# Optimization experiments

Measured on AMD Instinct MI355X. Metric: run time of the kernel, lower is better.

## Reference

```python
import math
import jax, jax.numpy as jnp
import numpy as np

WS = 16        # window size (square)
SHIFT = 8      # window_size // 2 (window_shift=True)
NUM_HEADS = 6

def _rel_coords_table(ws):
    # Swin-V2 log-spaced continuous relative coords, shape (1, 2ws-1, 2ws-1, 2)
    r = np.arange(-(ws - 1), ws, dtype=np.float32)
    t = np.stack(np.meshgrid(r, r, indexing='ij'), axis=-1)[None]
    t = t / (ws - 1) * 8.0
    t = np.sign(t) * np.log2(np.abs(t) + 1.0) / np.log2(8.0)
    return t.astype(np.float32)

def _rel_pos_index(ws):
    ch, cw = np.meshgrid(np.arange(ws), np.arange(ws), indexing='ij')
    coords = np.stack([ch.ravel(), cw.ravel()])          # (2, N)
    rel = coords[:, :, None] - coords[:, None, :]        # (2, N, N)
    rel = rel.transpose(1, 2, 0).astype(np.int64)
    rel[..., 0] += ws - 1
    rel[..., 1] += ws - 1
    rel[..., 0] *= 2 * ws - 1
    return rel.sum(-1).astype(np.int32)                  # (N, N), values in [0, (2ws-1)^2)

def _shift_mask(H, W, ws, shift):
    img = np.zeros((H, W), dtype=np.float32)
    cnt = 0
    for hs in (slice(0, -ws), slice(-ws, -shift), slice(-shift, None)):
        for wsl in (slice(0, -ws), slice(-ws, -shift), slice(-shift, None)):
            img[hs, wsl] = cnt; cnt += 1
    win = img.reshape(H // ws, ws, W // ws, ws).transpose(0, 2, 1, 3).reshape(-1, ws * ws)
    diff = win[:, None, :] - win[:, :, None]
    return np.where(diff != 0, -100.0, 0.0).astype(np.float32)  # (nW, N, N)

def setup_inputs():
    key = jax.random.key(0)
    ks = jax.random.split(key, 4)
    B, H, W = 16, 64, 64
    C = 3 * NUM_HEADS * 32  # 576 (qkv channels)
    qkv = jax.random.normal(ks[0], (B, H * W, C), dtype=jnp.float32)
    table = jnp.asarray(_rel_coords_table(WS))
    index = jnp.asarray(_rel_pos_index(WS))
    mask = jnp.asarray(_shift_mask(H, W, WS, SHIFT))
    logit_scale = jnp.log(10.0 * jnp.ones((NUM_HEADS, 1, 1), dtype=jnp.float32))
    w1 = jax.random.normal(ks[1], (512, 2), dtype=jnp.float32) * 0.02
    b1 = jnp.zeros((512,), dtype=jnp.float32)
    w2 = jax.random.normal(ks[2], (NUM_HEADS, 512), dtype=jnp.float32) * 0.02
    return {"qkv": qkv, "table": table, "mask": mask, "logit_scale": logit_scale,
            "w1": w1, "b1": b1, "w2": w2, "index": index, "H": H, "W": W}

def reference(qkv, table, mask, logit_scale, w1, b1, w2, index, H, W):
    B, L, C = qkv.shape
    dim = C // 3
    hd = dim // NUM_HEADS
    x = qkv.reshape(B, H, W, C)
    x = jnp.roll(x, (-SHIFT, -SHIFT), axis=(1, 2))
    nWh, nWw = H // WS, W // WS
    # window partition -> (B_, N, C)
    x = x.reshape(B, nWh, WS, nWw, WS, C).transpose(0, 1, 3, 2, 4, 5).reshape(-1, WS * WS, C)
    B_, N, _ = x.shape
    qkv_ = x.reshape(B_, N, 3, NUM_HEADS, hd).transpose(2, 0, 3, 1, 4)
    q, k, v = qkv_[0], qkv_[1], qkv_[2]  # (B_, H, N, hd)
    # cosine attention
    qn = q / jnp.maximum(jnp.linalg.norm(q, axis=-1, keepdims=True), 1e-12)
    kn = k / jnp.maximum(jnp.linalg.norm(k, axis=-1, keepdims=True), 1e-12)
    attn = jnp.einsum('bhnd,bhmd->bhnm', qn, kn)
    scale = jnp.exp(jnp.minimum(logit_scale, math.log(1.0 / 0.01)))  # (H,1,1)
    attn = attn * scale[None]
    # CPB MLP bias: Linear(2,512)+ReLU -> Linear(512,H,no bias)
    hidden = jax.nn.relu(table @ w1.T + b1)          # (1, 2ws-1, 2ws-1, 512)
    bias_table = (hidden @ w2.T).reshape(-1, NUM_HEADS)
    bias = bias_table[index.reshape(-1)].reshape(N, N, NUM_HEADS).transpose(2, 0, 1)
    attn = attn + 16.0 * jax.nn.sigmoid(bias)[None]
    # shifted-window mask
    nWm = mask.shape[0]
    attn = attn.reshape(B_ // nWm, nWm, NUM_HEADS, N, N) + mask[None, :, None]
    attn = attn.reshape(B_, NUM_HEADS, N, N)
    attn = jax.nn.softmax(attn, axis=-1)
    out = jnp.einsum('bhnm,bhmd->bhnd', attn, v)
    out = out.transpose(0, 2, 1, 3).reshape(B_, N, dim)
    # window reverse + unshift
    out = out.reshape(B, nWh, nWw, WS, WS, dim).transpose(0, 1, 3, 2, 4, 5).reshape(B, H, W, dim)
    out = jnp.roll(out, (SHIFT, SHIFT), axis=(1, 2))
    return out.reshape(B, L, dim)
```

## Files before the change

### kernel.cpp

```cpp
#include <hip/hip_runtime.h>
#include <cstdint>

#define NH 6
#define HD 32
#define NTOK 256
#define CIN 576
#define DIMO 192
#define LOG2E 1.44269504f
#define SHIFT2 37.6f
#define MNEG (-144.269504f)

typedef short short8 __attribute__((ext_vector_type(8)));
typedef float f32x4 __attribute__((ext_vector_type(4)));
typedef int   int4v __attribute__((ext_vector_type(4)));

__device__ __forceinline__ int grp6(int x) { return (x < 48) ? 0 : ((x < 56) ? 1 : 2); }

__device__ __forceinline__ unsigned short f2bf(float f) {
    unsigned int u = __float_as_uint(f);
    u += 0x7fffu + ((u >> 16) & 1u);
    return (unsigned short)(u >> 16);
}

__device__ __forceinline__ int qk_off(int tile, int row, int quad) {
    return tile * 512 + row * 32 + ((quad ^ ((row >> 1) & 3)) << 3);
}

__global__ void cpb_kernel(const float* __restrict__ table,
                           const float* __restrict__ w1,
                           const float* __restrict__ b1,
                           const float* __restrict__ w2,
                           float* __restrict__ bv) {
    __shared__ float hid[512];
    int p = blockIdx.x;
    float t0 = table[2 * p], t1 = table[2 * p + 1];
    int t = threadIdx.x;
    for (int j = t; j < 512; j += 256) {
        float hv = fmaf(t0, w1[2 * j], fmaf(t1, w1[2 * j + 1], b1[j]));
        hid[j] = fmaxf(hv, 0.f);
    }
    __syncthreads();
    if (t < 192) {
        int h = t >> 5, l = t & 31;
        const float* w2h = w2 + h * 512;
        float acc = 0.f;
        for (int j = l; j < 512; j += 32) acc = fmaf(hid[j], w2h[j], acc);
        acc += __shfl_xor(acc, 1, 32);
        acc += __shfl_xor(acc, 2, 32);
        acc += __shfl_xor(acc, 4, 32);
        acc += __shfl_xor(acc, 8, 32);
        acc += __shfl_xor(acc, 16, 32);
        if (l == 0) bv[h * 961 + p] = (16.f / (1.f + __expf(-acc))) * LOG2E - SHIFT2;
    }
}

__global__ __launch_bounds__(512, 4) void attn_kernel(
    const float* __restrict__ qkv,
    const float* __restrict__ logit_scale,
    const float* __restrict__ bv,
    float* __restrict__ out)
{
    __shared__ __align__(16) short Qb[NTOK * HD];
    __shared__ __align__(16) short Kb[NTOK * HD];
    __shared__ __align__(16) short Vt[HD * 264];
    __shared__ float Bv[961];

    const int t = threadIdx.x;
    const int h = blockIdx.x % NH;
    const int win = blockIdx.x / NH;
    const int b = win >> 4, wl = win & 15, wh = wl >> 2, ww = wl & 3;

    const float scale2 = __expf(fminf(logit_scale[h], 4.6051702f)) * LOG2E;

    for (int p = t; p < 961; p += 512) Bv[p] = bv[h * 961 + p];

    {
        if (t < 256) {
            int n = t;
            int i = n >> 4, j = n & 15;
            int rr = wh * 16 + i, cc = ww * 16 + j;
            int r = (rr + 8) & 63, c0 = (cc + 8) & 63;
            const float* base = qkv + ((long)(b * 4096 + r * 64 + c0)) * CIN + h * HD;
            float qv[32], kv[32];
            const float4* qp = (const float4*)base;
            const float4* kp = (const float4*)(base + DIMO);
#pragma unroll
            for (int w = 0; w < 8; ++w) {
                float4 x = qp[w];
                qv[4 * w + 0] = x.x; qv[4 * w + 1] = x.y; qv[4 * w + 2] = x.z; qv[4 * w + 3] = x.w;
            }
#pragma unroll
            for (int w = 0; w < 8; ++w) {
                float4 x = kp[w];
                kv[4 * w + 0] = x.x; kv[4 * w + 1] = x.y; kv[4 * w + 2] = x.z; kv[4 * w + 3] = x.w;
            }
            float sq = 0.f, sk = 0.f;
#pragma unroll
            for (int d = 0; d < 32; ++d) { sq = fmaf(qv[d], qv[d], sq); sk = fmaf(kv[d], kv[d], sk); }
            float qs = scale2 / fmaxf(sqrtf(sq), 1e-12f);
            float ks = 1.f / fmaxf(sqrtf(sk), 1e-12f);
#pragma unroll
            for (int w = 0; w < 4; ++w) {
                short8 qc, kc;
#pragma unroll
                for (int e = 0; e < 8; ++e) {
                    qc[e] = (short)f2bf(qv[8 * w + e] * qs);
                    kc[e] = (short)f2bf(kv[8 * w + e] * ks);
                }
                int off = qk_off(i, j, w);
                *(short8*)&Qb[off] = qc;
                *(short8*)&Kb[off] = kc;
            }
        } else {
            int n2 = t - 256;
            int m = n2 & 127, dh = n2 >> 7;
            int i = m >> 3;
            int ja = (2 * m) & 15;
            int r  = (wh * 16 + i + 8) & 63;
            int ca = (ww * 16 + ja + 8) & 63;
            int cb = (ww * 16 + ja + 1 + 8) & 63;
            const float* ba = qkv + ((long)(b * 4096 + r * 64 + ca)) * CIN + h * HD + 2 * DIMO + dh * 16;
            const float* bb = qkv + ((long)(b * 4096 + r * 64 + cb)) * CIN + h * HD + 2 * DIMO + dh * 16;
            float va[16], vb[16];
            const float4* pa4 = (const float4*)ba;
            const float4* pb4 = (const float4*)bb;
#pragma unroll
            for (int w = 0; w < 4; ++w) {
                float4 A = pa4[w], B = pb4[w];
                va[4 * w + 0] = A.x; va[4 * w + 1] = A.y; va[4 * w + 2] = A.z; va[4 * w + 3] = A.w;
                vb[4 * w + 0] = B.x; vb[4 * w + 1] = B.y; vb[4 * w + 2] = B.z; vb[4 * w + 3] = B.w;
            }
            int u = m & 15;
            int jp = ((u & 1) << 3) | ((u & 2) << 1) | ((u & 4) >> 1) | ((u & 8) >> 3);
            int colb = (m >> 4) * 32 + 2 * jp;
#pragma unroll
            for (int di = 0; di < 16; ++di) {
                unsigned pa_ = f2bf(va[di]);
                unsigned pb_ = f2bf(vb[di]);
                *(unsigned*)&Vt[(dh * 16 + di) * 264 + colb] = pa_ | (pb_ << 16);
            }
        }
    }
    __syncthreads();

    const int wv = t >> 6, lane = t & 63, quad = lane >> 4, l15 = lane & 15;

    int trg[2] = {wv * 2, wv * 2 + 1};
    short8 bQ[2];
#pragma unroll
    for (int tl = 0; tl < 2; ++tl)
        bQ[tl] = *(const short8*)&Qb[qk_off(trg[tl], l15, quad)];

    int gqr[2];
#pragma unroll
    for (int tl = 0; tl < 2; ++tl) gqr[tl] = grp6(wh * 16 + trg[tl]);
    const int gcl = grp6(ww * 16 + l15);
    float cm[4];
#pragma unroll
    for (int reg = 0; reg < 4; ++reg)
        cm[reg] = (gcl == grp6(ww * 16 + quad * 4 + reg)) ? 0.f : MNEG;

    f32x4 O[2][2];
    float lp[2] = {0.f, 0.f};
#pragma unroll
    for (int tl = 0; tl < 2; ++tl)
#pragma unroll
        for (int dtk = 0; dtk < 2; ++dtk) O[tl][dtk] = (f32x4){0.f, 0.f, 0.f, 0.f};

    const f32x4 Zero = (f32x4){0.f, 0.f, 0.f, 0.f};

    for (int c = 0; c < 8; ++c) {
        int ctg[2] = {2 * c, 2 * c + 1};
        short8 aK[2], bV[2];
#pragma unroll
        for (int ct = 0; ct < 2; ++ct)
            aK[ct] = *(const short8*)&Kb[qk_off(ctg[ct], l15, quad)];
#pragma unroll
        for (int dtk = 0; dtk < 2; ++dtk)
            bV[dtk] = *(const short8*)&Vt[(dtk * 16 + l15) * 264 + c * 32 + quad * 8];

        f32x4 S[2][2];
#pragma unroll
        for (int tl = 0; tl < 2; ++tl)
#pragma unroll
            for (int ct = 0; ct < 2; ++ct)
                S[tl][ct] = __builtin_amdgcn_mfma_f32_16x16x32_bf16(aK[ct], bQ[tl], Zero, 0, 0, 0);

        int gkr[2] = {grp6(wh * 16 + ctg[0]), grp6(wh * 16 + ctg[1])};

#pragma unroll
        for (int tl = 0; tl < 2; ++tl) {
            float ev[2][4];
#pragma unroll
            for (int ct = 0; ct < 2; ++ct) {
                int rb = (trg[tl] - ctg[ct] + 15) * 31 + 15 + l15 - 4 * quad;
                bool rmatch = (gqr[tl] == gkr[ct]);
#pragma unroll
                for (int reg = 0; reg < 4; ++reg) {
                    float madd = rmatch ? cm[reg] : MNEG;
                    float arg = S[tl][ct][reg] + (Bv[rb - reg] + madd);
                    float e = __builtin_amdgcn_exp2f(arg);
                    ev[ct][reg] = e;
                    lp[tl] += e;
                }
            }
            int p0, p1, p2, p3;
            asm("v_cvt_pk_bf16_f32 %0, %1, %2" : "=v"(p0) : "v"(ev[0][0]), "v"(ev[0][1]));
            asm("v_cvt_pk_bf16_f32 %0, %1, %2" : "=v"(p1) : "v"(ev[1][0]), "v"(ev[1][1]));
            asm("v_cvt_pk_bf16_f32 %0, %1, %2" : "=v"(p2) : "v"(ev[0][2]), "v"(ev[0][3]));
            asm("v_cvt_pk_bf16_f32 %0, %1, %2" : "=v"(p3) : "v"(ev[1][2]), "v"(ev[1][3]));
            asm("v_permlane32_swap_b32 %0, %1" : "+v"(p0), "+v"(p2));
            asm("v_permlane32_swap_b32 %0, %1" : "+v"(p1), "+v"(p3));
            int4v w = {p0, p1, p2, p3};
            union { int4v i; short8 s; } cvt; cvt.i = w;
            short8 aP = cvt.s;
            O[tl][0] = __builtin_amdgcn_mfma_f32_16x16x32_bf16(aP, bV[0], O[tl][0], 0, 0, 0);
            O[tl][1] = __builtin_amdgcn_mfma_f32_16x16x32_bf16(aP, bV[1], O[tl][1], 0, 0, 0);
        }
    }

    const long pixb = (long)b * 4096;
#pragma unroll
    for (int tl = 0; tl < 2; ++tl) {
        float s = lp[tl];
        s += __shfl_xor(s, 16);
        s += __shfl_xor(s, 32);
        float invf = 1.f / s;
        int r = (wh * 16 + trg[tl] + 8) & 63;
#pragma unroll
        for (int reg = 0; reg < 4; ++reg) {
            float iv = __shfl(invf, quad * 4 + reg);
            int cpix = (ww * 16 + quad * 4 + reg + 8) & 63;
            float* op = out + (pixb + r * 64 + cpix) * DIMO + h * HD + l15;
            op[0]  = O[tl][0][reg] * iv;
            op[16] = O[tl][1][reg] * iv;
        }
    }
}

extern "C" void kernel_launch(void* const* d_in, const int* in_sizes, int n_in,
                              void* d_out, int out_size, void* d_ws, size_t ws_size,
                              hipStream_t stream) {
    const float* qkv         = (const float*)d_in[0];
    const float* table       = (const float*)d_in[1];
    const float* logit_scale = (const float*)d_in[3];
    const float* w1          = (const float*)d_in[4];
    const float* b1          = (const float*)d_in[5];
    const float* w2          = (const float*)d_in[6];
    float* out = (float*)d_out;
    float* bv  = (float*)d_ws;

    cpb_kernel<<<961, 256, 0, stream>>>(table, w1, b1, w2, bv);
    attn_kernel<<<256 * NH, 512, 0, stream>>>(qkv, logit_scale, bv, out);
}
```

Before: 261.4 us.

## Remap block order for L2 locality and balance Q/K/V staging across all threads

Block index decoding is permuted so consecutive blocks cover different heads and windows of nearby rows, which is meant to improve L2/cache reuse of the shared qkv rows across the six heads. The staging phase is rebalanced: each thread now handles either Q or K of one token plus half of its V, instead of half the threads doing both Q and K and the other half doing V pairs. This evens out per-thread load and register pressure. The V transpose now writes individual 16-bit values with a rotated index, which may add shared-memory store instructions or bank conflicts.

New measurement: 262.7 us. About the same (+0.5%).

```diff
diff --git a/kernel.cpp b/kernel.cpp
--- a/kernel.cpp
+++ b/kernel.cpp
@@ -66,78 +66,72 @@
     __shared__ float Bv[961];
 
     const int t = threadIdx.x;
-    const int h = blockIdx.x % NH;
-    const int win = blockIdx.x / NH;
-    const int b = win >> 4, wl = win & 15, wh = wl >> 2, ww = wl & 3;
+
+    const int id  = blockIdx.x;
+    const int r8  = id & 7, q3 = id >> 3;
+    const int j24 = q3 % 24, g8 = q3 / 24;
+    const int gg  = r8 + 8 * g8;
+    const int h   = j24 % 6, ww = j24 / 6;
+    const int wh  = gg & 3,  b  = gg >> 2;
 
     const float scale2 = __expf(fminf(logit_scale[h], 4.6051702f)) * LOG2E;
 
     for (int p = t; p < 961; p += 512) Bv[p] = bv[h * 961 + p];
 
     {
-        if (t < 256) {
-            int n = t;
-            int i = n >> 4, j = n & 15;
-            int rr = wh * 16 + i, cc = ww * 16 + j;
-            int r = (rr + 8) & 63, c0 = (cc + 8) & 63;
-            const float* base = qkv + ((long)(b * 4096 + r * 64 + c0)) * CIN + h * HD;
-            float qv[32], kv[32];
-            const float4* qp = (const float4*)base;
-            const float4* kp = (const float4*)(base + DIMO);
+        const int n = t >> 1, s = t & 1;
+        const int i = n >> 4, j = n & 15;
+        const int rr = (wh * 16 + i + 8) & 63;
+        const int cc = (ww * 16 + j + 8) & 63;
+        const float* base = qkv + ((long)(b * 4096 + rr * 64 + cc)) * CIN + h * HD;
+
+        float xv[32];
+        {
+            const float4* p4 = (const float4*)(base + s * DIMO);
 #pragma unroll
             for (int w = 0; w < 8; ++w) {
-                float4 x = qp[w];
-                qv[4 * w + 0] = x.x; qv[4 * w + 1] = x.y; qv[4 * w + 2] = x.z; qv[4 * w + 3] = x.w;
-            }
-#pragma unroll
-            for (int w = 0; w < 8; ++w) {
-                float4 x = kp[w];
-                kv[4 * w + 0] = x.x; kv[4 * w + 1] = x.y; kv[4 * w + 2] = x.z; kv[4 * w + 3] = x.w;
-            }
-            float sq = 0.f, sk = 0.f;
-#pragma unroll
-            for (int d = 0; d < 32; ++d) { sq = fmaf(qv[d], qv[d], sq); sk = fmaf(kv[d], kv[d], sk); }
-            float qs = scale2 / fmaxf(sqrtf(sq), 1e-12f);
-            float ks = 1.f / fmaxf(sqrtf(sk), 1e-12f);
+                float4 x = p4[w];
+                xv[4 * w + 0] = x.x; xv[4 * w + 1] = x.y; xv[4 * w + 2] = x.z; xv[4 * w + 3] = x.w;
+            }
+        }
+        float vv[16];
+        {
+            const float4* v4 = (const float4*)(base + 2 * DIMO + s * 16);
 #pragma unroll
             for (int w = 0; w < 4; ++w) {
-                short8 qc, kc;
-#pragma unroll
-                for (int e = 0; e < 8; ++e) {
-                    qc[e] = (short)f2bf(qv[8 * w + e] * qs);
-                    kc[e] = (short)f2bf(kv[8 * w + e] * ks);
-                }
-                int off = qk_off(i, j, w);
-                *(short8*)&Qb[off] = qc;
-                *(short8*)&Kb[off] = kc;
-            }
-        } else {
-            int n2 = t - 256;
-            int m = n2 & 127, dh = n2 >> 7;
-            int i = m >> 3;
-            int ja = (2 * m) & 15;
-            int r  = (wh * 16 + i + 8) & 63;
-            int ca = (ww * 16 + ja + 8) & 63;
-            int cb = (ww * 16 + ja + 1 + 8) & 63;
-            const float* ba = qkv + ((long)(b * 4096 + r * 64 + ca)) * CIN + h * HD + 2 * DIMO + dh * 16;
-            const float* bb = qkv + ((long)(b * 4096 + r * 64 + cb)) * CIN + h * HD + 2 * DIMO + dh * 16;
-            float va[16], vb[16];
-            const float4* pa4 = (const float4*)ba;
-            const float4* pb4 = (const float4*)bb;
-#pragma unroll
-            for (int w = 0; w < 4; ++w) {
-                float4 A = pa4[w], B = pb4[w];
-                va[4 * w + 0] = A.x; va[4 * w + 1] = A.y; va[4 * w + 2] = A.z; va[4 * w + 3] = A.w;
-                vb[4 * w + 0] = B.x; vb[4 * w + 1] = B.y; vb[4 * w + 2] = B.z; vb[4 * w + 3] = B.w;
-            }
-            int u = m & 15;
+                float4 x = v4[w];
+                vv[4 * w + 0] = x.x; vv[4 * w + 1] = x.y; vv[4 * w + 2] = x.z; vv[4 * w + 3] = x.w;
+            }
+        }
+
+        float a0 = 0.f, a1 = 0.f, a2 = 0.f, a3 = 0.f;
+#pragma unroll
+        for (int d = 0; d < 8; ++d) {
+            a0 = fmaf(xv[d],      xv[d],      a0);
+            a1 = fmaf(xv[d + 8],  xv[d + 8],  a1);
+            a2 = fmaf(xv[d + 16], xv[d + 16], a2);
+            a3 = fmaf(xv[d + 24], xv[d + 24], a3);
+        }
+        float ssum = (a0 + a1) + (a2 + a3);
+        float sc = (s ? 1.f : scale2) / fmaxf(sqrtf(ssum), 1e-12f);
+
+        short* dst = s ? Kb : Qb;
+#pragma unroll
+        for (int w = 0; w < 4; ++w) {
+            short8 xc;
+#pragma unroll
+            for (int e = 0; e < 8; ++e) xc[e] = (short)f2bf(xv[8 * w + e] * sc);
+            *(short8*)&dst[qk_off(i, j, w)] = xc;
+        }
+
+        {
+            int u = (n >> 1) & 15;
             int jp = ((u & 1) << 3) | ((u & 2) << 1) | ((u & 4) >> 1) | ((u & 8) >> 3);
-            int colb = (m >> 4) * 32 + 2 * jp;
+            int col = (n >> 5) * 32 + 2 * jp + (n & 1);
 #pragma unroll
             for (int di = 0; di < 16; ++di) {
-                unsigned pa_ = f2bf(va[di]);
-                unsigned pb_ = f2bf(vb[di]);
-                *(unsigned*)&Vt[(dh * 16 + di) * 264 + colb] = pa_ | (pb_ << 16);
+                int e = (di + 4 * s) & 15;
+                Vt[(s * 16 + e) * 264 + col] = (short)f2bf(vv[e]);
             }
         }
     }
```
